# Kernel optimization log

Hardware: AMD Instinct MI355X
Metric: run time of the kernel (lower is better)

## Reference

```python
import jax, jax.numpy as jnp
import numpy as np

DELTA = 0.2  # margin from __init__
EPS = 1e-8   # torch cosine_similarity eps


def setup_inputs() -> dict:
    key = jax.random.key(0)
    k1, k2, k3 = jax.random.split(key, 3)
    B, D, N = 4096, 1024, 8192
    return {
        "q": jax.random.normal(k1, (B, D), dtype=jnp.float32),
        "k": jax.random.normal(k2, (B, D), dtype=jnp.float32),
        "queue": jax.random.normal(k3, (N, D), dtype=jnp.float32),
    }


def _l2_normalize(x):
    # matches torch cosine_similarity clamping: norm clamped to eps
    n = jnp.maximum(jnp.linalg.norm(x, axis=-1, keepdims=True), EPS)
    return x / n


def reference(q, k, queue):
    qn = _l2_normalize(q)          # [B, D]
    kn = _l2_normalize(k)          # [B, D]
    queuen = _l2_normalize(queue)  # [N, D]
    pos = jnp.sum(qn * kn, axis=-1)                 # [B] cos(q_i, k_i)
    neg = jnp.einsum("bd,nd->bn", qn, queuen)       # [B, N] cos(q_i, queue_j)
    hinge = jax.nn.relu(DELTA - pos[:, None] + neg)  # [B, N]
    return jnp.sum(hinge)
```

## Files before the change

### kernel.cpp

```cpp
#include <hip/hip_runtime.h>

#define B_ROWS 4096
#define N_ROWS 8192
#define DDIM   1024
#define DELTA_M 0.2f
#define EPSF    1e-8f

#define BK3 32
#define NW  (DDIM / BK3)

typedef short bf16x8 __attribute__((ext_vector_type(8)));
typedef float f32x4 __attribute__((ext_vector_type(4)));

__device__ inline unsigned short f32_to_bf16(float f) {
    unsigned int u = __float_as_uint(f);
    u += 0x7FFFu + ((u >> 16) & 1u);
    return (unsigned short)(u >> 16);
}

__device__ inline void load_lds16(const void* g, void* l) {
    __builtin_amdgcn_global_load_lds(
        (const __attribute__((address_space(1))) void*)g,
        (__attribute__((address_space(3))) void*)l,
        16, 0, 0);
}

__global__ __launch_bounds__(256)
void norm_kernel(const float* __restrict__ q, const float* __restrict__ k,
                 const float* __restrict__ queue,
                 unsigned short* __restrict__ qn,
                 unsigned short* __restrict__ qun,
                 float* __restrict__ pos, float* __restrict__ out) {
    const int tid  = threadIdx.x;
    const int lane = tid & 63;
    const int wave = tid >> 6;
    const int row  = blockIdx.x * 4 + wave;
    if (blockIdx.x == 0 && tid == 0) *out = 0.f;

    if (row < B_ROWS) {
        const float4* qr = reinterpret_cast<const float4*>(q + (size_t)row * DDIM);
        const float4* kr = reinterpret_cast<const float4*>(k + (size_t)row * DDIM);
        float4 a[4], b[4];
        #pragma unroll
        for (int j = 0; j < 4; ++j) a[j] = qr[lane + j * 64];
        #pragma unroll
        for (int j = 0; j < 4; ++j) b[j] = kr[lane + j * 64];
        float s11 = 0.f, s22 = 0.f, s12 = 0.f;
        #pragma unroll
        for (int j = 0; j < 4; ++j) {
            s11 += a[j].x * a[j].x + a[j].y * a[j].y + a[j].z * a[j].z + a[j].w * a[j].w;
            s22 += b[j].x * b[j].x + b[j].y * b[j].y + b[j].z * b[j].z + b[j].w * b[j].w;
            s12 += a[j].x * b[j].x + a[j].y * b[j].y + a[j].z * b[j].z + a[j].w * b[j].w;
        }
        #pragma unroll
        for (int off = 1; off < 64; off <<= 1) {
            s11 += __shfl_xor(s11, off);
            s22 += __shfl_xor(s22, off);
            s12 += __shfl_xor(s12, off);
        }
        const float inv1 = 1.0f / fmaxf(sqrtf(s11), EPSF);
        const float inv2 = 1.0f / fmaxf(sqrtf(s22), EPSF);
        if (lane == 0) pos[row] = s12 * inv1 * inv2;
        ushort4* orow = reinterpret_cast<ushort4*>(qn + (size_t)row * DDIM);
        #pragma unroll
        for (int j = 0; j < 4; ++j) {
            ushort4 o;
            o.x = f32_to_bf16(a[j].x * inv1);
            o.y = f32_to_bf16(a[j].y * inv1);
            o.z = f32_to_bf16(a[j].z * inv1);
            o.w = f32_to_bf16(a[j].w * inv1);
            orow[lane + j * 64] = o;
        }
    } else {
        const int r2 = row - B_ROWS;
        const float4* qr = reinterpret_cast<const float4*>(queue + (size_t)r2 * DDIM);
        float4 a[4];
        #pragma unroll
        for (int j = 0; j < 4; ++j) a[j] = qr[lane + j * 64];
        float s11 = 0.f;
        #pragma unroll
        for (int j = 0; j < 4; ++j)
            s11 += a[j].x * a[j].x + a[j].y * a[j].y + a[j].z * a[j].z + a[j].w * a[j].w;
        #pragma unroll
        for (int off = 1; off < 64; off <<= 1) s11 += __shfl_xor(s11, off);
        const float inv1 = 1.0f / fmaxf(sqrtf(s11), EPSF);
        ushort4* orow = reinterpret_cast<ushort4*>(qun + (size_t)r2 * DDIM);
        #pragma unroll
        for (int j = 0; j < 4; ++j) {
            ushort4 o;
            o.x = f32_to_bf16(a[j].x * inv1);
            o.y = f32_to_bf16(a[j].y * inv1);
            o.z = f32_to_bf16(a[j].z * inv1);
            o.w = f32_to_bf16(a[j].w * inv1);
            orow[lane + j * 64] = o;
        }
    }
}

__device__ __forceinline__ void stage_pair(const unsigned short* srcA,
                                           const unsigned short* srcB,
                                           int k0, unsigned char* bufA, int t16) {
    load_lds16(srcA + k0, bufA + t16);
    load_lds16(srcB + k0, bufA + 16384 + t16);
}

template<bool STG, int WE>
__device__ __forceinline__ void gemm_window(
    int T, unsigned char* lds,
    const unsigned short* srcA, const unsigned short* srcB,
    int aBase, int bBase, int t16, f32x4 (&acc)[4][4]) {

    const int par = T & 1;
    unsigned char* buf = lds + par * 32768;

    bf16x8 a[4], b[4];
    #pragma unroll
    for (int fm = 0; fm < 4; ++fm)
        a[fm] = *reinterpret_cast<const bf16x8*>(&buf[aBase + fm * 1024]);
    #pragma unroll
    for (int fn = 0; fn < 4; ++fn)
        b[fn] = *reinterpret_cast<const bf16x8*>(&buf[16384 + bBase + fn * 1024]);
    asm volatile("s_waitcnt lgkmcnt(0)" ::: "memory");
    __builtin_amdgcn_sched_barrier(0);
    __builtin_amdgcn_s_barrier();

    if (STG)
        stage_pair(srcA, srcB, (T + 2) * BK3, buf, t16);

    __builtin_amdgcn_s_setprio(1);
    #pragma unroll
    for (int fm = 0; fm < 4; ++fm)
        #pragma unroll
        for (int fn = 0; fn < 4; ++fn)
            acc[fm][fn] = __builtin_amdgcn_mfma_f32_16x16x32_bf16(
                a[fm], b[fn], acc[fm][fn], 0, 0, 0);
    __builtin_amdgcn_s_setprio(0);

    if (WE >= 0) {
        if (WE == 2)      asm volatile("s_waitcnt vmcnt(2)" ::: "memory");
        else              asm volatile("s_waitcnt vmcnt(0)" ::: "memory");
        __builtin_amdgcn_sched_barrier(0);
        __builtin_amdgcn_s_barrier();
    }
}

__global__ __launch_bounds__(1024, 4)
void gemm_hinge(const unsigned short* __restrict__ A,
                const unsigned short* __restrict__ Bq,
                const float* __restrict__ pos,
                float* __restrict__ out) {
    __shared__ __align__(16) unsigned char lds[65536];

    const int tid  = threadIdx.x;
    const int lane = tid & 63;
    const int wave = tid >> 6;

    const int bid = blockIdx.x;
    const int x   = bid & 7;
    const int idx = bid >> 3;
    const int bm = ((x & 1) * 8 + (idx & 7)) * 256;
    const int bn = ((x >> 1) * 8 + (idx >> 3)) * 256;

    const int wr = wave >> 2, wc = wave & 3;
    const int ln15 = lane & 15, kq = lane >> 4;
    const int kqoff = (kq * 16) ^ (((ln15 >> 1) & 3) << 4);
    const int aBase = (wr * 64 + ln15) * 64 + kqoff;
    const int bBase = (wc * 64 + ln15) * 64 + kqoff;

    const int t16 = tid * 16;
    const int l   = t16 ^ (((t16 >> 7) & 3) << 4);
    const int sr  = l >> 6;
    const int sc  = (l & 63) >> 1;
    const unsigned short* srcA = A  + (size_t)(bm + sr) * DDIM + sc;
    const unsigned short* srcB = Bq + (size_t)(bn + sr) * DDIM + sc;

    f32x4 acc[4][4];
    #pragma unroll
    for (int fm = 0; fm < 4; ++fm)
        #pragma unroll
        for (int fn = 0; fn < 4; ++fn)
            acc[fm][fn] = (f32x4){0.f, 0.f, 0.f, 0.f};

    stage_pair(srcA, srcB, 0,   lds,         t16);
    stage_pair(srcA, srcB, BK3, lds + 32768, t16);
    asm volatile("s_waitcnt vmcnt(2)" ::: "memory");
    __builtin_amdgcn_sched_barrier(0);
    __builtin_amdgcn_s_barrier();

    #pragma unroll 1
    for (int T = 0; T < NW - 2; ++T)
        gemm_window<true, 2>(T, lds, srcA, srcB, aBase, bBase, t16, acc);
    gemm_window<false, 0>(NW - 2, lds, srcA, srcB, aBase, bBase, t16, acc);
    gemm_window<false, -1>(NW - 1, lds, srcA, srcB, aBase, bBase, t16, acc);

    float lsum = 0.f;
    #pragma unroll
    for (int fm = 0; fm < 4; ++fm) {
        const float4 p4 = *reinterpret_cast<const float4*>(
            pos + bm + wr * 64 + fm * 16 + kq * 4);
        const float pj[4] = {p4.x, p4.y, p4.z, p4.w};
        #pragma unroll
        for (int fn = 0; fn < 4; ++fn)
            #pragma unroll
            for (int j = 0; j < 4; ++j)
                lsum += fmaxf(DELTA_M - pj[j] + acc[fm][fn][j], 0.f);
    }
    #pragma unroll
    for (int off = 32; off; off >>= 1) lsum += __shfl_down(lsum, off);
    __syncthreads();
    float* red = reinterpret_cast<float*>(lds);
    if (lane == 0) red[wave] = lsum;
    __syncthreads();
    if (tid == 0) {
        float s = 0.f;
        #pragma unroll
        for (int w = 0; w < 16; ++w) s += red[w];
        atomicAdd(out, s);
    }
}

extern "C" void kernel_launch(void* const* d_in, const int* in_sizes, int n_in,
                              void* d_out, int out_size, void* d_ws, size_t ws_size,
                              hipStream_t stream) {
    const float* q     = (const float*)d_in[0];
    const float* k     = (const float*)d_in[1];
    const float* queue = (const float*)d_in[2];
    float* out = (float*)d_out;

    unsigned short* qn  = (unsigned short*)d_ws;
    unsigned short* qun = qn + (size_t)B_ROWS * DDIM;
    float* pos = (float*)(qun + (size_t)N_ROWS * DDIM);

    norm_kernel<<<(B_ROWS + N_ROWS) / 4, 256, 0, stream>>>(q, k, queue, qn, qun, pos, out);
    gemm_hinge<<<(B_ROWS / 256) * (N_ROWS / 256), 1024, 0, stream>>>(qn, qun, pos, out);
}
```

Baseline: 162.7 us.

## Use 512-thread blocks with 8x4 MFMA tiles and triple-buffered LDS pipeline

Halves the GEMM block to 8 waves, each computing a 128x64 sub-tile (8x4 MFMA fragments), so every wave reuses its B fragments across more A rows. LDS grows to three 32KB stages with prefetch three windows ahead, and fragments for the next window are register double-buffered so LDS reads overlap the current MFMAs. Only one barrier per window remains. The cost is higher register pressure (32 accumulators plus two fragment sets) and lower occupancy from 96KB of LDS per block.

```diff
diff --git a/kernel.cpp b/kernel.cpp
--- a/kernel.cpp
+++ b/kernel.cpp
@@ -97,59 +97,62 @@
     }
 }
 
-__device__ __forceinline__ void stage_pair(const unsigned short* srcA,
-                                           const unsigned short* srcB,
-                                           int k0, unsigned char* bufA, int t16) {
-    load_lds16(srcA + k0, bufA + t16);
-    load_lds16(srcB + k0, bufA + 16384 + t16);
+struct Frags { bf16x8 a[8]; bf16x8 b[4]; };
+
+__device__ __forceinline__ void ld_frags(const unsigned char* buf, int aBase, int bBase,
+                                         Frags& f) {
+    #pragma unroll
+    for (int fm = 0; fm < 8; ++fm)
+        f.a[fm] = *reinterpret_cast<const bf16x8*>(&buf[aBase + fm * 1024]);
+    #pragma unroll
+    for (int fn = 0; fn < 4; ++fn)
+        f.b[fn] = *reinterpret_cast<const bf16x8*>(&buf[16384 + bBase + fn * 1024]);
+}
+
+__device__ __forceinline__ void do_mfma(const Frags& f, f32x4 (&acc)[8][4]) {
+    __builtin_amdgcn_s_setprio(1);
+    #pragma unroll
+    for (int fm = 0; fm < 8; ++fm)
+        #pragma unroll
+        for (int fn = 0; fn < 4; ++fn)
+            acc[fm][fn] = __builtin_amdgcn_mfma_f32_16x16x32_bf16(
+                f.a[fm], f.b[fn], acc[fm][fn], 0, 0, 0);
+    __builtin_amdgcn_s_setprio(0);
+}
+
+__device__ __forceinline__ void stage(const unsigned short* sA0, const unsigned short* sA1,
+                                      const unsigned short* sB0, const unsigned short* sB1,
+                                      int k0, unsigned char* buf, int t16) {
+    load_lds16(sA0 + k0, buf + t16);
+    load_lds16(sA1 + k0, buf + 8192 + t16);
+    load_lds16(sB0 + k0, buf + 16384 + t16);
+    load_lds16(sB1 + k0, buf + 24576 + t16);
 }
 
 template<bool STG, int WE>
-__device__ __forceinline__ void gemm_window(
-    int T, unsigned char* lds,
-    const unsigned short* srcA, const unsigned short* srcB,
-    int aBase, int bBase, int t16, f32x4 (&acc)[4][4]) {
-
-    const int par = T & 1;
-    unsigned char* buf = lds + par * 32768;
-
-    bf16x8 a[4], b[4];
-    #pragma unroll
-    for (int fm = 0; fm < 4; ++fm)
-        a[fm] = *reinterpret_cast<const bf16x8*>(&buf[aBase + fm * 1024]);
-    #pragma unroll
-    for (int fn = 0; fn < 4; ++fn)
-        b[fn] = *reinterpret_cast<const bf16x8*>(&buf[16384 + bBase + fn * 1024]);
+__device__ __forceinline__ void window(int T, unsigned char* lds,
+    Frags& use, Frags& nxt,
+    const unsigned short* sA0, const unsigned short* sA1,
+    const unsigned short* sB0, const unsigned short* sB1,
+    int aBase, int bBase, int t16, f32x4 (&acc)[8][4]) {
+
+    ld_frags(lds + ((T + 1) % 3) * 32768, aBase, bBase, nxt);
+    if (STG)
+        stage(sA0, sA1, sB0, sB1, (T + 3) * BK3, lds + (T % 3) * 32768, t16);
+    do_mfma(use, acc);
+    if (WE == 4)      asm volatile("s_waitcnt vmcnt(4)" ::: "memory");
+    else if (WE == 0) asm volatile("s_waitcnt vmcnt(0)" ::: "memory");
     asm volatile("s_waitcnt lgkmcnt(0)" ::: "memory");
     __builtin_amdgcn_sched_barrier(0);
-    __builtin_amdgcn_s_barrier();
-
-    if (STG)
-        stage_pair(srcA, srcB, (T + 2) * BK3, buf, t16);
-
-    __builtin_amdgcn_s_setprio(1);
-    #pragma unroll
-    for (int fm = 0; fm < 4; ++fm)
-        #pragma unroll
-        for (int fn = 0; fn < 4; ++fn)
-            acc[fm][fn] = __builtin_amdgcn_mfma_f32_16x16x32_bf16(
-                a[fm], b[fn], acc[fm][fn], 0, 0, 0);
-    __builtin_amdgcn_s_setprio(0);
-
-    if (WE >= 0) {
-        if (WE == 2)      asm volatile("s_waitcnt vmcnt(2)" ::: "memory");
-        else              asm volatile("s_waitcnt vmcnt(0)" ::: "memory");
-        __builtin_amdgcn_sched_barrier(0);
-        __builtin_amdgcn_s_barrier();
-    }
-}
-
-__global__ __launch_bounds__(1024, 4)
+    if (WE >= 0) __builtin_amdgcn_s_barrier();
+}
+
+__global__ __launch_bounds__(512, 2)
 void gemm_hinge(const unsigned short* __restrict__ A,
                 const unsigned short* __restrict__ Bq,
                 const float* __restrict__ pos,
                 float* __restrict__ out) {
-    __shared__ __align__(16) unsigned char lds[65536];
+    __shared__ __align__(16) unsigned char lds[98304];
 
     const int tid  = threadIdx.x;
     const int lane = tid & 63;
@@ -164,40 +167,55 @@
     const int wr = wave >> 2, wc = wave & 3;
     const int ln15 = lane & 15, kq = lane >> 4;
     const int kqoff = (kq * 16) ^ (((ln15 >> 1) & 3) << 4);
-    const int aBase = (wr * 64 + ln15) * 64 + kqoff;
-    const int bBase = (wc * 64 + ln15) * 64 + kqoff;
+    const int aBase = wr * 8192 + ln15 * 64 + kqoff;
+    const int bBase = wc * 4096 + ln15 * 64 + kqoff;
 
     const int t16 = tid * 16;
-    const int l   = t16 ^ (((t16 >> 7) & 3) << 4);
-    const int sr  = l >> 6;
-    const int sc  = (l & 63) >> 1;
-    const unsigned short* srcA = A  + (size_t)(bm + sr) * DDIM + sc;
-    const unsigned short* srcB = Bq + (size_t)(bn + sr) * DDIM + sc;
-
-    f32x4 acc[4][4];
-    #pragma unroll
-    for (int fm = 0; fm < 4; ++fm)
+    const int d0 = t16, d1 = t16 + 8192;
+    const int l0 = d0 ^ (((d0 >> 7) & 3) << 4);
+    const int l1 = d1 ^ (((d1 >> 7) & 3) << 4);
+    const int sr0 = l0 >> 6, sc0 = (l0 & 63) >> 1;
+    const int sr1 = l1 >> 6, sc1 = (l1 & 63) >> 1;
+    const unsigned short* sA0 = A  + (size_t)(bm + sr0) * DDIM + sc0;
+    const unsigned short* sA1 = A  + (size_t)(bm + sr1) * DDIM + sc1;
+    const unsigned short* sB0 = Bq + (size_t)(bn + sr0) * DDIM + sc0;
+    const unsigned short* sB1 = Bq + (size_t)(bn + sr1) * DDIM + sc1;
+
+    f32x4 acc[8][4];
+    #pragma unroll
+    for (int fm = 0; fm < 8; ++fm)
         #pragma unroll
         for (int fn = 0; fn < 4; ++fn)
             acc[fm][fn] = (f32x4){0.f, 0.f, 0.f, 0.f};
 
-    stage_pair(srcA, srcB, 0,   lds,         t16);
-    stage_pair(srcA, srcB, BK3, lds + 32768, t16);
-    asm volatile("s_waitcnt vmcnt(2)" ::: "memory");
+    Frags fA, fB;
+
+    stage(sA0, sA1, sB0, sB1, 0,       lds,         t16);
+    stage(sA0, sA1, sB0, sB1, BK3,     lds + 32768, t16);
+    stage(sA0, sA1, sB0, sB1, 2 * BK3, lds + 65536, t16);
+    asm volatile("s_waitcnt vmcnt(8)" ::: "memory");
     __builtin_amdgcn_sched_barrier(0);
     __builtin_amdgcn_s_barrier();
+    ld_frags(lds, aBase, bBase, fA);
+    asm volatile("s_waitcnt vmcnt(4) lgkmcnt(0)" ::: "memory");
+    __builtin_amdgcn_sched_barrier(0);
+    __builtin_amdgcn_s_barrier();
 
     #pragma unroll 1
-    for (int T = 0; T < NW - 2; ++T)
-        gemm_window<true, 2>(T, lds, srcA, srcB, aBase, bBase, t16, acc);
-    gemm_window<false, 0>(NW - 2, lds, srcA, srcB, aBase, bBase, t16, acc);
-    gemm_window<false, -1>(NW - 1, lds, srcA, srcB, aBase, bBase, t16, acc);
+    for (int T = 0; T < 28; T += 2) {
+        window<true, 4>(T,     lds, fA, fB, sA0, sA1, sB0, sB1, aBase, bBase, t16, acc);
+        window<true, 4>(T + 1, lds, fB, fA, sA0, sA1, sB0, sB1, aBase, bBase, t16, acc);
+    }
+    window<true,  4>(28, lds, fA, fB, sA0, sA1, sB0, sB1, aBase, bBase, t16, acc);
+    window<false, 0>(29, lds, fB, fA, sA0, sA1, sB0, sB1, aBase, bBase, t16, acc);
+    window<false,-1>(30, lds, fA, fB, sA0, sA1, sB0, sB1, aBase, bBase, t16, acc);
+    do_mfma(fB, acc);
 
     float lsum = 0.f;
     #pragma unroll
-    for (int fm = 0; fm < 4; ++fm) {
+    for (int fm = 0; fm < 8; ++fm) {
         const float4 p4 = *reinterpret_cast<const float4*>(
-            pos + bm + wr * 64 + fm * 16 + kq * 4);
+            pos + bm + wr * 128 + fm * 16 + kq * 4);
         const float pj[4] = {p4.x, p4.y, p4.z, p4.w};
         #pragma unroll
         for (int fn = 0; fn < 4; ++fn)
@@ -214,7 +232,7 @@
     if (tid == 0) {
         float s = 0.f;
         #pragma unroll
-        for (int w = 0; w < 16; ++w) s += red[w];
+        for (int w = 0; w < 8; ++w) s += red[w];
         atomicAdd(out, s);
     }
 }
@@ -232,5 +250,5 @@
     float* pos = (float*)(qun + (size_t)N_ROWS * DDIM);
 
     norm_kernel<<<(B_ROWS + N_ROWS) / 4, 256, 0, stream>>>(q, k, queue, qn, qun, pos, out);
-    gemm_hinge<<<(B_ROWS / 256) * (N_ROWS / 256), 1024, 0, stream>>>(qn, qun, pos, out);
-}
+    gemm_hinge<<<(B_ROWS / 256) * (N_ROWS / 256), 512, 0, stream>>>(qn, qun, pos, out);
+}
```

Measured after the change: 155.4 us. 1.05x faster.
